# Performance work log

Measured on AMD Instinct MI355X. Metric: run time of the kernel, lower is better.

The kernel has to match this reference:

```python
import jax, jax.numpy as jnp
import numpy as np

H, DH, M, ITERS = 8, 64, 256, 6   # heads, dim_head, num_landmarks, pinv iters
DIM = H * DH                      # 512
KERNEL = 33                       # residual depthwise conv kernel


def setup_inputs() -> dict:
    key = jax.random.key(0)
    ks = jax.random.split(key, 5)
    b, n = 2, 8192                # n multiple of M -> no divisibility padding
    x = jax.random.normal(ks[0], (b, n, DIM), jnp.float32)
    ln_gamma = jnp.ones((DIM,), jnp.float32)
    ln_beta = jnp.zeros((DIM,), jnp.float32)
    w_qkv = jax.random.normal(ks[1], (DIM, 3 * DIM), jnp.float32) * 0.02
    w_out = jax.random.normal(ks[2], (DIM, DIM), jnp.float32) * 0.02
    b_out = jnp.zeros((DIM,), jnp.float32)
    res_kernel = jax.random.normal(ks[3], (H, 1, KERNEL, 1), jnp.float32) * 0.02
    return {"x": x, "ln_gamma": ln_gamma, "ln_beta": ln_beta, "w_qkv": w_qkv,
            "w_out": w_out, "b_out": b_out, "res_kernel": res_kernel}


def _pinv(a, iters):
    # lucidrains moore_penrose_iter_pinv (Newton-Schulz iteration)
    abs_a = jnp.abs(a)
    scale = abs_a.sum(-1).max() * abs_a.sum(-2).max()
    z = jnp.swapaxes(a, -1, -2) / scale
    I = jnp.eye(a.shape[-1], dtype=a.dtype)
    for _ in range(iters):
        az = a @ z
        z = 0.25 * z @ (13.0 * I - az @ (15.0 * I - az @ (7.0 * I - az)))
    return z


def reference(x, ln_gamma, ln_beta, w_qkv, w_out, b_out, res_kernel):
    b, n, d = x.shape
    # pre-LayerNorm (eps 1e-5)
    mu = jnp.mean(x, -1, keepdims=True)
    var = jnp.var(x, -1, keepdims=True)
    xn = (x - mu) * jax.lax.rsqrt(var + 1e-5) * ln_gamma + ln_beta
    # qkv projection (bias-free)
    q, k, v = jnp.split(xn @ w_qkv, 3, axis=-1)
    to_heads = lambda t: t.reshape(b, n, H, DH).transpose(0, 2, 1, 3)  # b h n d
    q, k, v = to_heads(q), to_heads(k), to_heads(v)
    q = q * (DH ** -0.5)
    # landmarks: mean over groups of l consecutive tokens ('(m l) d -> m d')
    l = n // M
    q_l = q.reshape(b, H, M, l, DH).mean(3)  # b h M d
    k_l = k.reshape(b, H, M, l, DH).mean(3)
    sim1 = jnp.einsum('bhnd,bhmd->bhnm', q, k_l)      # queries vs k-landmarks
    sim2 = jnp.einsum('bhid,bhjd->bhij', q_l, k_l)    # landmarks vs landmarks
    sim3 = jnp.einsum('bhmd,bhnd->bhmn', q_l, k)      # q-landmarks vs keys
    a1 = jax.nn.softmax(sim1, axis=-1)
    a2 = jax.nn.softmax(sim2, axis=-1)
    a3 = jax.nn.softmax(sim3, axis=-1)
    a2_inv = _pinv(a2, ITERS)
    out = (a1 @ a2_inv) @ (a3 @ v)  # b h n d
    # residual depthwise conv over the sequence axis (Conv2d kernel (33,1), groups=H)
    pad = KERNEL // 2
    out = out + jax.lax.conv_general_dilated(
        v, res_kernel, (1, 1), [(pad, pad), (0, 0)],
        dimension_numbers=('NCHW', 'OIHW', 'NCHW'), feature_group_count=H)
    out = out.transpose(0, 2, 1, 3).reshape(b, n, d)
    out = out @ w_out + b_out  # to_out Linear (dropout inactive at eval)
    return x + out             # TransLayer residual
```

## Files before the change

kernel.cpp:

```cpp
#include <hip/hip_runtime.h>
#include <math.h>

#define H_ 8
#define DH_ 64
#define DIM_ 512
#define M_ 256
#define N_ 8192
#define BH_ 16
#define LG_ 32
#define KC_ 33
#define PADC_ 16

typedef __attribute__((ext_vector_type(8))) short bf16x8;
typedef __attribute__((ext_vector_type(4))) short s16x4;
typedef __attribute__((ext_vector_type(4))) float f32x4;

__device__ __forceinline__ short f2bf(float f) {
  unsigned u = __float_as_uint(f);
  unsigned r = (u + 0x7FFF + ((u >> 16) & 1)) >> 16;
  return (short)r;
}
__device__ __forceinline__ float bf2f(short s) {
  return __uint_as_float(((unsigned)(unsigned short)s) << 16);
}

__device__ __forceinline__ void mfma_nt_core(const short* __restrict__ A,
                                             const short* __restrict__ Bt, int K,
                                             int m0, int n0, size_t lda, size_t ldb,
                                             f32x4 acc[4][4], short* As, short* Bs) {
  const int tid = threadIdx.x;
  const int wave = tid >> 6, lane = tid & 63;
  const int wr = (wave >> 1) * 64, wc = (wave & 1) * 64;
  const int mi = lane & 15, quad = lane >> 4;
  for (int k0 = 0; k0 < K; k0 += 32) {
#pragma unroll
    for (int t = 0; t < 2; ++t) {
      const int cbase = (t * 4 + wave) * 64;
      const int chunk = cbase + lane;
      const int row = chunk >> 2, cc = (chunk & 3) * 8;
      __builtin_amdgcn_global_load_lds(
          (const __attribute__((address_space(1))) void*)(A + (size_t)(m0 + row) * lda + k0 + cc),
          (__attribute__((address_space(3))) void*)(As + (size_t)cbase * 8), 16, 0, 0);
      __builtin_amdgcn_global_load_lds(
          (const __attribute__((address_space(1))) void*)(Bt + (size_t)(n0 + row) * ldb + k0 + cc),
          (__attribute__((address_space(3))) void*)(Bs + (size_t)cbase * 8), 16, 0, 0);
    }
    __syncthreads();
    bf16x8 af[4], bf[4];
#pragma unroll
    for (int i = 0; i < 4; ++i)
      af[i] = *(const bf16x8*)&As[(wr + i * 16 + mi) * 32 + quad * 8];
#pragma unroll
    for (int j = 0; j < 4; ++j)
      bf[j] = *(const bf16x8*)&Bs[(wc + j * 16 + mi) * 32 + quad * 8];
#pragma unroll
    for (int i = 0; i < 4; ++i)
#pragma unroll
      for (int j = 0; j < 4; ++j)
        acc[i][j] = __builtin_amdgcn_mfma_f32_16x16x32_bf16(af[i], bf[j], acc[i][j], 0, 0, 0);
    __syncthreads();
  }
}

__global__ __launch_bounds__(256) void qkv_mfma(const short* __restrict__ xnb,
                                                const short* __restrict__ wt,
                                                short* __restrict__ qb, short* __restrict__ kb,
                                                short* __restrict__ vb) {
  __shared__ short As[128 * 32], Bs[128 * 32];
  f32x4 acc[4][4] = {};
  const int m0 = blockIdx.x * 128, n0 = blockIdx.y * 128;
  mfma_nt_core(xnb, wt, DIM_, m0, n0, DIM_, DIM_, acc, As, Bs);
  const int wave = threadIdx.x >> 6, lane = threadIdx.x & 63;
  const int wr = (wave >> 1) * 64, wc = (wave & 1) * 64;
  const int mi = lane & 15, quad = lane >> 4;
  const int which = n0 >> 9;
  short* dst = which == 0 ? qb : which == 1 ? kb : vb;
  const float sc = which == 0 ? 0.125f : 1.0f;
#pragma unroll
  for (int j = 0; j < 4; ++j) {
    const int col = n0 + wc + j * 16 + mi;
    const int h = (col >> 6) & 7, d = col & 63;
#pragma unroll
    for (int i = 0; i < 4; ++i) {
#pragma unroll
      for (int r = 0; r < 4; ++r) {
        const int row = m0 + wr + i * 16 + quad * 4 + r;
        const int b = row >> 13, t = row & (N_ - 1);
        dst[((size_t)(b * H_ + h) * N_ + t) * DH_ + d] = f2bf(acc[i][j][r] * sc);
      }
    }
  }
}

__global__ __launch_bounds__(256) void final_mfma(const short* __restrict__ omb,
                                                  const short* __restrict__ wt,
                                                  const float* __restrict__ x,
                                                  const float* __restrict__ bout,
                                                  float* __restrict__ y) {
  __shared__ short As[128 * 32], Bs[128 * 32];
  f32x4 acc[4][4] = {};
  const int m0 = blockIdx.x * 128, n0 = blockIdx.y * 128;
  mfma_nt_core(omb, wt, DIM_, m0, n0, DIM_, DIM_, acc, As, Bs);
  const int wave = threadIdx.x >> 6, lane = threadIdx.x & 63;
  const int wr = (wave >> 1) * 64, wc = (wave & 1) * 64;
  const int mi = lane & 15, quad = lane >> 4;
#pragma unroll
  for (int j = 0; j < 4; ++j) {
    const int col = n0 + wc + j * 16 + mi;
    const float bo = bout[col];
#pragma unroll
    for (int i = 0; i < 4; ++i) {
#pragma unroll
      for (int r = 0; r < 4; ++r) {
        const int row = m0 + wr + i * 16 + quad * 4 + r;
        y[(size_t)row * DIM_ + col] = acc[i][j][r] + x[(size_t)row * DIM_ + col] + bo;
      }
    }
  }
}

__global__ __launch_bounds__(256) void convt_kernel(const float* __restrict__ in,
                                                    short* __restrict__ out, int K, int N) {
  __shared__ float tile[32][33];
  const int n0 = blockIdx.x * 32, k0 = blockIdx.y * 32;
  const int tx = threadIdx.x & 31, ty = threadIdx.x >> 5;
  for (int r = ty; r < 32; r += 8) tile[r][tx] = in[(size_t)(k0 + r) * N + n0 + tx];
  __syncthreads();
  for (int r = ty; r < 32; r += 8) out[(size_t)(n0 + r) * K + k0 + tx] = f2bf(tile[tx][r]);
}

__global__ __launch_bounds__(256) void vt_kernel(const short* __restrict__ vb,
                                                 short* __restrict__ vtb) {
  __shared__ short tile[32][33];
  const int t0 = blockIdx.x * 32, d0 = blockIdx.y * 32, bh = blockIdx.z;
  const int tx = threadIdx.x & 31, ty = threadIdx.x >> 5;
  for (int r = ty; r < 32; r += 8)
    tile[r][tx] = vb[((size_t)bh * N_ + t0 + r) * DH_ + d0 + tx];
  __syncthreads();
  for (int r = ty; r < 32; r += 8)
    vtb[((size_t)bh * DH_ + d0 + r) * N_ + t0 + tx] = tile[tx][r];
}

__global__ __launch_bounds__(128) void ln_kernel(const float* __restrict__ x,
                                                 const float* __restrict__ gamma,
                                                 const float* __restrict__ beta,
                                                 short* __restrict__ xnb) {
  const int row = blockIdx.x, tid = threadIdx.x;
  const float4 v = ((const float4*)(x + (size_t)row * DIM_))[tid];
  float s = v.x + v.y + v.z + v.w;
  float ss = v.x * v.x + v.y * v.y + v.z * v.z + v.w * v.w;
  __shared__ float r1[128], r2[128];
  r1[tid] = s;
  r2[tid] = ss;
  __syncthreads();
  for (int off = 64; off > 0; off >>= 1) {
    if (tid < off) {
      r1[tid] += r1[tid + off];
      r2[tid] += r2[tid + off];
    }
    __syncthreads();
  }
  const float mu = r1[0] * (1.0f / DIM_);
  const float var = r2[0] * (1.0f / DIM_) - mu * mu;
  const float rs = rsqrtf(var + 1e-5f);
  const float4 g = ((const float4*)gamma)[tid];
  const float4 bb = ((const float4*)beta)[tid];
  s16x4 o = {f2bf((v.x - mu) * rs * g.x + bb.x), f2bf((v.y - mu) * rs * g.y + bb.y),
             f2bf((v.z - mu) * rs * g.z + bb.z), f2bf((v.w - mu) * rs * g.w + bb.w)};
  ((s16x4*)(xnb + (size_t)row * DIM_))[tid] = o;
}

__global__ __launch_bounds__(256) void landmark_kernel(const short* __restrict__ qb,
                                                       const short* __restrict__ kb,
                                                       float* __restrict__ ql,
                                                       float* __restrict__ kl,
                                                       short* __restrict__ qlb,
                                                       short* __restrict__ klb) {
  const int idx = blockIdx.x * 256 + threadIdx.x;
  const int d = idx & (DH_ - 1);
  const int m = (idx >> 6) & (M_ - 1);
  const int bh = idx >> 14;
  const size_t base = ((size_t)bh * N_ + m * LG_) * DH_ + d;
  float sq = 0.f, sk = 0.f;
#pragma unroll 8
  for (int t = 0; t < LG_; ++t) {
    sq += bf2f(qb[base + (size_t)t * DH_]);
    sk += bf2f(kb[base + (size_t)t * DH_]);
  }
  sq *= (1.0f / LG_);
  sk *= (1.0f / LG_);
  ql[idx] = sq;
  kl[idx] = sk;
  qlb[idx] = f2bf(sq);
  klb[idx] = f2bf(sk);
}

__global__ __launch_bounds__(256) void sim2_softmax(const float* __restrict__ ql,
                                                    const float* __restrict__ kl,
                                                    float* __restrict__ a2,
                                                    short* __restrict__ a2b) {
  const int i = blockIdx.x, bh = blockIdx.y, j = threadIdx.x;
  __shared__ float qrow[DH_];
  if (j < DH_) qrow[j] = ql[((size_t)bh * M_ + i) * DH_ + j];
  __syncthreads();
  const float* kr = kl + ((size_t)bh * M_ + j) * DH_;
  float s = 0.f;
#pragma unroll 16
  for (int d = 0; d < DH_; ++d) s += qrow[d] * kr[d];
  __shared__ float red[256];
  red[j] = s;
  __syncthreads();
  for (int off = 128; off > 0; off >>= 1) {
    if (j < off) red[j] = fmaxf(red[j], red[j + off]);
    __syncthreads();
  }
  const float mx = red[0];
  __syncthreads();
  const float e = expf(s - mx);
  red[j] = e;
  __syncthreads();
  for (int off = 128; off > 0; off >>= 1) {
    if (j < off) red[j] += red[j + off];
    __syncthreads();
  }
  const float out = e / red[0];
  a2[((size_t)bh * M_ + i) * M_ + j] = out;
  a2b[((size_t)bh * M_ + i) * M_ + j] = f2bf(out);
}

__global__ __launch_bounds__(256) void colmax_kernel(const float* __restrict__ a2,
                                                     unsigned int* __restrict__ scalebits) {
  const int bh = blockIdx.x, j = threadIdx.x;
  const float* mat = a2 + (size_t)bh * M_ * M_;
  float s = 0.f;
  for (int i = 0; i < M_; ++i) s += fabsf(mat[i * M_ + j]);
  __shared__ float red[256];
  red[j] = s;
  __syncthreads();
  for (int off = 128; off > 0; off >>= 1) {
    if (j < off) red[j] = fmaxf(red[j], red[j + off]);
    __syncthreads();
  }
  if (j == 0) atomicMax(scalebits, __float_as_uint(red[0]));
}

__global__ __launch_bounds__(256) void transpose_scale(const float* __restrict__ a2,
                                                       short* __restrict__ z0b,
                                                       const unsigned int* __restrict__ scalebits) {
  const float inv = 1.0f / __uint_as_float(*scalebits);
  const int idx = blockIdx.x * 256 + threadIdx.x;
  const int j = idx & (M_ - 1), i = (idx >> 8) & (M_ - 1), bh = idx >> 16;
  z0b[idx] = f2bf(a2[((size_t)bh * M_ + j) * M_ + i] * inv);
}

__device__ __forceinline__ void ns_core(const short* __restrict__ A, const short* __restrict__ B,
                                        int m0, int n0, short* As, short* Bs, f32x4 acc[4]) {
  const int tid = threadIdx.x, wave = tid >> 6, lane = tid & 63;
  const int mi = lane & 15, quad = lane >> 4;
  const int arow = tid >> 2, acol = (tid & 3) * 8;
  const int bkk = tid & 31, g = tid >> 5;
  for (int k0 = 0; k0 < M_; k0 += 32) {
    __builtin_amdgcn_global_load_lds(
        (const __attribute__((address_space(1))) void*)(A + (size_t)(m0 + arow) * M_ + k0 + acol),
        (__attribute__((address_space(3))) void*)(As + (size_t)wave * 512), 16, 0, 0);
    const bf16x8 bv = *(const bf16x8*)(B + (size_t)(k0 + bkk) * M_ + n0 + g * 8);
#pragma unroll
    for (int e = 0; e < 8; ++e) Bs[(g * 8 + e) * 44 + bkk] = bv[e];
    __syncthreads();
    const bf16x8 af = *(const bf16x8*)&As[(wave * 16 + mi) * 32 + quad * 8];
#pragma unroll
    for (int j = 0; j < 4; ++j) {
      union { bf16x8 v; s16x4 h[2]; } bfr;
      const short* bp = &Bs[(j * 16 + mi) * 44 + quad * 8];
      bfr.h[0] = *(const s16x4*)bp;
      bfr.h[1] = *(const s16x4*)(bp + 4);
      acc[j] = __builtin_amdgcn_mfma_f32_16x16x32_bf16(af, bfr.v, acc[j], 0, 0, 0);
    }
    __syncthreads();
  }
}

__device__ __forceinline__ int ns_remap() {
  const int lin = blockIdx.y * 16 + blockIdx.x;
  return (lin & 7) * (gridDim.y << 1) + (lin >> 3);
}

__global__ __launch_bounds__(256) void ns_gemm0(const short* __restrict__ A,
                                                const short* __restrict__ B,
                                                short* __restrict__ C) {
  __shared__ short As[64 * 32], Bs[64 * 44];
  const int id = ns_remap();
  const int bx = id & 15, by = id >> 4;
  const int m0 = (bx >> 2) * 64, n0 = (bx & 3) * 64;
  const size_t mo = (size_t)by * (M_ * M_);
  f32x4 acc[4] = {};
  ns_core(A + mo, B + mo, m0, n0, As, Bs, acc);
  const int wave = threadIdx.x >> 6, lane = threadIdx.x & 63;
  const int mi = lane & 15, quad = lane >> 4;
#pragma unroll
  for (int j = 0; j < 4; ++j)
#pragma unroll
    for (int r = 0; r < 4; ++r) {
      const int row = m0 + wave * 16 + quad * 4 + r, col = n0 + j * 16 + mi;
      C[mo + (size_t)row * M_ + col] = f2bf(acc[j][r]);
    }
}

__global__ __launch_bounds__(256) void ns_stageA(const short* __restrict__ z,
                                                 const short* __restrict__ y,
                                                 short* __restrict__ p1,
                                                 short* __restrict__ y2,
                                                 short* __restrict__ w) {
  __shared__ short As[64 * 32], Bs[64 * 44];
  const int id = ns_remap();
  const int bx = id & 15, by = id >> 4;
  const int m0 = (bx >> 2) * 64, n0 = (bx & 3) * 64;
  const int sel = by & 1;
  const size_t mo = (size_t)(by >> 1) * (M_ * M_);
  f32x4 acc[4] = {};
  ns_core((sel ? y : z) + mo, y + mo, m0, n0, As, Bs, acc);
  const int wave = threadIdx.x >> 6, lane = threadIdx.x & 63;
  const int mi = lane & 15, quad = lane >> 4;
#pragma unroll
  for (int j = 0; j < 4; ++j)
#pragma unroll
    for (int r = 0; r < 4; ++r) {
      const int row = m0 + wave * 16 + quad * 4 + r, col = n0 + j * 16 + mi;
      const size_t idx = mo + (size_t)row * M_ + col;
      if (sel) {
        y2[idx] = f2bf(acc[j][r]);
        w[idx] = f2bf(1.75f * bf2f(y[idx]) - 0.25f * acc[j][r]);
      } else {
        p1[idx] = f2bf(acc[j][r]);
      }
    }
}

__global__ __launch_bounds__(256) void ns_stageB(const short* __restrict__ p1,
                                                 const short* __restrict__ y2,
                                                 const short* __restrict__ w,
                                                 const short* __restrict__ z,
                                                 const short* __restrict__ y,
                                                 short* __restrict__ zo,
                                                 short* __restrict__ yo,
                                                 float* __restrict__ zf, int zonly) {
  __shared__ short As[64 * 32], Bs[64 * 44];
  const int id = ns_remap();
  const int bx = id & 15, by = id >> 4;
  const int m0 = (bx >> 2) * 64, n0 = (bx & 3) * 64;
  const int sel = zonly ? 0 : (by & 1);
  const size_t mo = (size_t)(zonly ? by : (by >> 1)) * (M_ * M_);
  f32x4 acc[4] = {};
  ns_core((sel ? y2 : p1) + mo, w + mo, m0, n0, As, Bs, acc);
  const int wave = threadIdx.x >> 6, lane = threadIdx.x & 63;
  const int mi = lane & 15, quad = lane >> 4;
#pragma unroll
  for (int j = 0; j < 4; ++j)
#pragma unroll
    for (int r = 0; r < 4; ++r) {
      const int row = m0 + wave * 16 + quad * 4 + r, col = n0 + j * 16 + mi;
      const size_t idx = mo + (size_t)row * M_ + col;
      if (sel) {
        yo[idx] = f2bf(3.25f * bf2f(y[idx]) - 3.75f * bf2f(y2[idx]) + acc[j][r]);
      } else {
        const float v = 3.25f * bf2f(z[idx]) - 3.75f * bf2f(p1[idx]) + acc[j][r];
        zo[idx] = f2bf(v);
        if (zf) zf[idx] = v;
      }
    }
}

__device__ __forceinline__ void mm_step(float (*As)[68], float (*Bs)[68],
                                        int tr, int tc, float acc[4][4]) {
#pragma unroll
  for (int kk = 0; kk < 16; ++kk) {
    const float4 a4 = *(const float4*)&As[kk][tr * 4];
    const float4 b4 = *(const float4*)&Bs[kk][tc * 4];
    const float a[4] = {a4.x, a4.y, a4.z, a4.w};
    const float b[4] = {b4.x, b4.y, b4.z, b4.w};
#pragma unroll
    for (int i = 0; i < 4; ++i)
#pragma unroll
      for (int j = 0; j < 4; ++j) acc[i][j] = fmaf(a[i], b[j], acc[i][j]);
  }
}

__device__ __forceinline__ void load_a_tile(const float* A, int lda, int m0, int k0,
                                            int tid, float (*As)[68]) {
  const int r = tid >> 2, kq = tid & 3;
  const float4 a4 = *(const float4*)(A + (size_t)(m0 + r) * lda + k0 + kq * 4);
  As[kq * 4 + 0][r] = a4.x;
  As[kq * 4 + 1][r] = a4.y;
  As[kq * 4 + 2][r] = a4.z;
  As[kq * 4 + 3][r] = a4.w;
}

__device__ __forceinline__ void load_b_nn(const float* B, int ldb, int k0, int n0,
                                          int tid, float (*Bs)[68]) {
  const int kr = tid >> 4, c4 = tid & 15;
  const float4 b4 = *(const float4*)(B + (size_t)(k0 + kr) * ldb + n0 + c4 * 4);
  *(float4*)&Bs[kr][c4 * 4] = b4;
}

__global__ __launch_bounds__(256) void gemm_nn64(const float* __restrict__ A, int lda,
                                                 long long strideA,
                                                 const float* __restrict__ B, long long strideB,
                                                 float* __restrict__ C, long long strideC,
                                                 int kchunk) {
  const int bz = blockIdx.z;
  A += (size_t)bz * strideA;
  B += (size_t)bz * strideB;
  C += (size_t)bz * strideC;
  const int m0 = blockIdx.x * 64;
  const int tid = threadIdx.x, tr = tid >> 4, tc = tid & 15;
  __shared__ float As[16][68], Bs[16][68];
  float acc[4][4] = {};
  for (int k0 = 0; k0 < kchunk; k0 += 16) {
    load_a_tile(A, lda, m0, k0, tid, As);
    load_b_nn(B, DH_, k0, 0, tid, Bs);
    __syncthreads();
    mm_step(As, Bs, tr, tc, acc);
    __syncthreads();
  }
#pragma unroll
  for (int i = 0; i < 4; ++i) {
    const int row = m0 + tr * 4 + i;
    *(float4*)(C + (size_t)row * DH_ + tc * 4) =
        make_float4(acc[i][0], acc[i][1], acc[i][2], acc[i][3]);
  }
}

__global__ __launch_bounds__(256) void a3_flash(const short* __restrict__ qlb,
                                                const short* __restrict__ kb,
                                                const short* __restrict__ vtb,
                                                float* __restrict__ Opart,
                                                float* __restrict__ mpart,
                                                float* __restrict__ lpart) {
  const int chunk = blockIdx.x, rt = blockIdx.y, bh = blockIdx.z;
  __shared__ short qs[64 * 80], ks[64 * 80], ps[64 * 80];
  const int tid = threadIdx.x, wave = tid >> 6, lane = tid & 63;
  const int mi = lane & 15, quad = lane >> 4;
#pragma unroll
  for (int i = 0; i < 2; ++i) {
    const int c = tid * 2 + i, row = c >> 3, col = (c & 7) * 8;
    *(bf16x8*)&qs[row * 80 + col] =
        *(const bf16x8*)(qlb + ((size_t)bh * M_ + rt * 64 + row) * DH_ + col);
  }
  __syncthreads();
  const bf16x8 aq0 = *(const bf16x8*)&qs[(wave * 16 + mi) * 80 + quad * 8];
  const bf16x8 aq1 = *(const bf16x8*)&qs[(wave * 16 + mi) * 80 + 32 + quad * 8];
  float m[4] = {-INFINITY, -INFINITY, -INFINITY, -INFINITY};
  float l[4] = {0.f, 0.f, 0.f, 0.f};
  f32x4 o[4] = {};
  for (int t = 0; t < 16; ++t) {
    const int n0 = chunk * 1024 + t * 64;
#pragma unroll
    for (int i = 0; i < 2; ++i) {
      const int c = tid * 2 + i, row = c >> 3, col = (c & 7) * 8;
      *(bf16x8*)&ks[row * 80 + col] =
          *(const bf16x8*)(kb + ((size_t)bh * N_ + n0 + row) * DH_ + col);
    }
    __syncthreads();
    f32x4 s[4];
#pragma unroll
    for (int j = 0; j < 4; ++j) {
      const bf16x8 b0 = *(const bf16x8*)&ks[(j * 16 + mi) * 80 + quad * 8];
      const bf16x8 b1 = *(const bf16x8*)&ks[(j * 16 + mi) * 80 + 32 + quad * 8];
      f32x4 z = {0.f, 0.f, 0.f, 0.f};
      z = __builtin_amdgcn_mfma_f32_16x16x32_bf16(aq0, b0, z, 0, 0, 0);
      s[j] = __builtin_amdgcn_mfma_f32_16x16x32_bf16(aq1, b1, z, 0, 0, 0);
    }
    float alpha[4];
#pragma unroll
    for (int r = 0; r < 4; ++r) {
      float v = fmaxf(fmaxf(s[0][r], s[1][r]), fmaxf(s[2][r], s[3][r]));
      v = fmaxf(v, __shfl_xor(v, 1, 64));
      v = fmaxf(v, __shfl_xor(v, 2, 64));
      v = fmaxf(v, __shfl_xor(v, 4, 64));
      v = fmaxf(v, __shfl_xor(v, 8, 64));
      const float mnew = fmaxf(m[r], v);
      alpha[r] = __expf(m[r] - mnew);
      m[r] = mnew;
    }
    float rs[4] = {0.f, 0.f, 0.f, 0.f};
#pragma unroll
    for (int j = 0; j < 4; ++j)
#pragma unroll
      for (int r = 0; r < 4; ++r) {
        const float p = __expf(s[j][r] - m[r]);
        rs[r] += p;
        ps[(wave * 16 + quad * 4 + r) * 80 + j * 16 + mi] = f2bf(p);
      }
#pragma unroll
    for (int r = 0; r < 4; ++r) {
      float v = rs[r];
      v += __shfl_xor(v, 1, 64);
      v += __shfl_xor(v, 2, 64);
      v += __shfl_xor(v, 4, 64);
      v += __shfl_xor(v, 8, 64);
      l[r] = l[r] * alpha[r] + v;
#pragma unroll
      for (int j = 0; j < 4; ++j) o[j][r] *= alpha[r];
    }
    __syncthreads();
    const bf16x8 ap0 = *(const bf16x8*)&ps[(wave * 16 + mi) * 80 + quad * 8];
    const bf16x8 ap1 = *(const bf16x8*)&ps[(wave * 16 + mi) * 80 + 32 + quad * 8];
#pragma unroll
    for (int j = 0; j < 4; ++j) {
      const short* vp = vtb + ((size_t)bh * DH_ + j * 16 + mi) * N_ + n0;
      const bf16x8 b0 = *(const bf16x8*)(vp + quad * 8);
      const bf16x8 b1 = *(const bf16x8*)(vp + 32 + quad * 8);
      o[j] = __builtin_amdgcn_mfma_f32_16x16x32_bf16(ap0, b0, o[j], 0, 0, 0);
      o[j] = __builtin_amdgcn_mfma_f32_16x16x32_bf16(ap1, b1, o[j], 0, 0, 0);
    }
    __syncthreads();
  }
  const int p2 = bh * 4 + rt;
  float* Ob = Opart + ((size_t)chunk * 64 + p2) * 4096;
#pragma unroll
  for (int j = 0; j < 4; ++j)
#pragma unroll
    for (int r = 0; r < 4; ++r)
      Ob[(wave * 16 + quad * 4 + r) * 64 + j * 16 + mi] = o[j][r];
  if (mi == 0) {
#pragma unroll
    for (int r = 0; r < 4; ++r) {
      mpart[((size_t)chunk * 64 + p2) * 64 + wave * 16 + quad * 4 + r] = m[r];
      lpart[((size_t)chunk * 64 + p2) * 64 + wave * 16 + quad * 4 + r] = l[r];
    }
  }
}

__global__ __launch_bounds__(256) void a3_combine(const float* __restrict__ Opart,
                                                  const float* __restrict__ mpart,
                                                  const float* __restrict__ lpart,
                                                  float* __restrict__ a3v) {
  const int p2 = blockIdx.x;
  const int bh = p2 >> 2, rt = p2 & 3;
  __shared__ float wgt[8][64];
  const int tid = threadIdx.x;
  if (tid < 64) {
    float mg = -INFINITY;
    for (int c = 0; c < 8; ++c) mg = fmaxf(mg, mpart[((size_t)c * 64 + p2) * 64 + tid]);
    float e[8], lg = 0.f;
    for (int c = 0; c < 8; ++c) {
      e[c] = __expf(mpart[((size_t)c * 64 + p2) * 64 + tid] - mg);
      lg += lpart[((size_t)c * 64 + p2) * 64 + tid] * e[c];
    }
    const float inv = 1.f / lg;
    for (int c = 0; c < 8; ++c) wgt[c][tid] = e[c] * inv;
  }
  __syncthreads();
  for (int i = tid; i < 4096; i += 256) {
    const int row = i >> 6, d = i & 63;
    float s = 0.f;
    for (int c = 0; c < 8; ++c) s += Opart[((size_t)c * 64 + p2) * 4096 + i] * wgt[c][row];
    a3v[((size_t)bh * M_ + rt * 64 + row) * DH_ + d] = s;
  }
}

__global__ __launch_bounds__(256) void w2t_kernel(const float* __restrict__ w2,
                                                  short* __restrict__ w2tb) {
  const int bh = blockIdx.x, tid = threadIdx.x;
  for (int i = tid; i < M_ * DH_; i += 256) {
    const int r = i >> 6, d = i & 63;
    w2tb[((size_t)bh * DH_ + d) * M_ + r] = f2bf(w2[(size_t)bh * M_ * DH_ + i]);
  }
}

__global__ __launch_bounds__(256, 5) void a1_conv(const short* __restrict__ qb,
                                                  const short* __restrict__ klb,
                                                  const short* __restrict__ w2tb,
                                                  const short* __restrict__ vtb,
                                                  const float* __restrict__ rk,
                                                  short* __restrict__ omb) {
  __shared__ __align__(16) char smem[20096];
  short* kls = (short*)smem;
  short* ps = (short*)smem;
  short* vwin = (short*)smem;
  short* band = (short*)(smem + 17920);
  const int bh = blockIdx.y, t0 = blockIdx.x * 64;
  const int b = bh >> 3, h = bh & 7;
  const int tid = threadIdx.x, wave = tid >> 6, lane = tid & 63;
  const int mi = lane & 15, quad = lane >> 4;

  const short* qrow = qb + ((size_t)bh * N_ + t0 + wave * 16 + mi) * DH_;
  const bf16x8 aq0 = *(const bf16x8*)(qrow + quad * 8);
  const bf16x8 aq1 = *(const bf16x8*)(qrow + 32 + quad * 8);

#pragma unroll
  for (int i = 0; i < 4; ++i) {
    const int idx = tid + i * 256;
    const int r = idx >> 6, c = idx & 63, u = c - r;
    band[r * 68 + c] = (u >= 0 && u < KC_) ? f2bf(rk[h * KC_ + u]) : (short)0;
  }

  f32x4 s[16] = {};
#pragma unroll
  for (int half = 0; half < 2; ++half) {
    if (half) __syncthreads();
#pragma unroll
    for (int i = 0; i < 4; ++i) {
      const int cb = i * 256 + wave * 64;
      const int c = cb + lane;
      const int row = c >> 3, cc = c & 7;
      __builtin_amdgcn_global_load_lds(
          (const __attribute__((address_space(1))) void*)(
              klb + ((size_t)bh * M_ + half * 128 + row) * DH_ + (cc ^ (row & 7)) * 8),
          (__attribute__((address_space(3))) void*)(kls + (size_t)cb * 8), 16, 0, 0);
    }
    __syncthreads();
#pragma unroll
    for (int f = 0; f < 8; ++f) {
      const int row = f * 16 + mi;
      const bf16x8 blo = *(const bf16x8*)&kls[row * 64 + ((quad ^ (row & 7)) * 8)];
      const bf16x8 bhi = *(const bf16x8*)&kls[row * 64 + (((quad + 4) ^ (row & 7)) * 8)];
      f32x4 z = __builtin_amdgcn_mfma_f32_16x16x32_bf16(aq0, blo, s[half * 8 + f], 0, 0, 0);
      s[half * 8 + f] = __builtin_amdgcn_mfma_f32_16x16x32_bf16(aq1, bhi, z, 0, 0, 0);
    }
  }
  float inv[4];
#pragma unroll
  for (int r = 0; r < 4; ++r) {
    float v = s[0][r];
#pragma unroll
    for (int f = 1; f < 16; ++f) v = fmaxf(v, s[f][r]);
    v = fmaxf(v, __shfl_xor(v, 1, 64));
    v = fmaxf(v, __shfl_xor(v, 2, 64));
    v = fmaxf(v, __shfl_xor(v, 4, 64));
    v = fmaxf(v, __shfl_xor(v, 8, 64));
    float sum = 0.f;
#pragma unroll
    for (int f = 0; f < 16; ++f) {
      const float p = __expf(s[f][r] - v);
      s[f][r] = p;
      sum += p;
    }
    sum += __shfl_xor(sum, 1, 64);
    sum += __shfl_xor(sum, 2, 64);
    sum += __shfl_xor(sum, 4, 64);
    sum += __shfl_xor(sum, 8, 64);
    inv[r] = 1.f / sum;
  }
  __syncthreads();

  f32x4 o[4] = {};
#pragma unroll
  for (int half = 0; half < 2; ++half) {
#pragma unroll
    for (int f = 0; f < 8; ++f)
#pragma unroll
      for (int r = 0; r < 4; ++r)
        ps[(wave * 16 + quad * 4 + r) * 140 + f * 16 + mi] = f2bf(s[half * 8 + f][r] * inv[r]);
#pragma unroll
    for (int k0 = 0; k0 < 4; ++k0) {
      union { bf16x8 v; s16x4 hh[2]; } ap;
      const short* pp = &ps[(wave * 16 + mi) * 140 + k0 * 32 + quad * 8];
      ap.hh[0] = *(const s16x4*)pp;
      ap.hh[1] = *(const s16x4*)(pp + 4);
#pragma unroll
      for (int j = 0; j < 4; ++j) {
        const bf16x8 bw = *(const bf16x8*)(w2tb + ((size_t)bh * DH_ + j * 16 + mi) * M_ +
                                           (half * 4 + k0) * 32 + quad * 8);
        o[j] = __builtin_amdgcn_mfma_f32_16x16x32_bf16(ap.v, bw, o[j], 0, 0, 0);
      }
    }
  }
  __syncthreads();

  {
    const int d = tid & 63, cg0 = tid >> 6;
    const short* vrow = vtb + ((size_t)bh * DH_ + d) * N_;
    for (int ch = cg0; ch < 14; ch += 4) {
      const int tbase = t0 - 16 + ch * 8;
      bf16x8 vv;
      if (tbase >= 0 && tbase + 8 <= N_) {
        vv = *(const bf16x8*)(vrow + tbase);
      } else {
#pragma unroll
        for (int e = 0; e < 8; ++e) {
          const int tt = tbase + e;
          vv[e] = (tt >= 0 && tt < N_) ? vrow[tt] : (short)0;
        }
      }
      *(bf16x8*)&vwin[d * 116 + ch * 8] = vv;
    }
  }
  __syncthreads();

#pragma unroll
  for (int ks = 0; ks < 2; ++ks) {
    union { bf16x8 v; s16x4 hh[2]; } ab;
    const short* bp = &band[mi * 68 + ks * 32 + quad * 8];
    ab.hh[0] = *(const s16x4*)bp;
    ab.hh[1] = *(const s16x4*)(bp + 4);
#pragma unroll
    for (int j = 0; j < 4; ++j) {
      union { bf16x8 v; s16x4 hh[2]; } bv;
      const short* vp = &vwin[(j * 16 + mi) * 116 + wave * 16 + ks * 32 + quad * 8];
      bv.hh[0] = *(const s16x4*)vp;
      bv.hh[1] = *(const s16x4*)(vp + 4);
      o[j] = __builtin_amdgcn_mfma_f32_16x16x32_bf16(ab.v, bv.v, o[j], 0, 0, 0);
    }
  }
#pragma unroll
  for (int j = 0; j < 4; ++j) {
    const int d = j * 16 + mi;
#pragma unroll
    for (int r = 0; r < 4; ++r) {
      const int t = t0 + wave * 16 + quad * 4 + r;
      omb[((size_t)(b * N_ + t)) * DIM_ + h * DH_ + d] = f2bf(o[j][r]);
    }
  }
}

extern "C" void kernel_launch(void* const* d_in, const int* in_sizes, int n_in,
                              void* d_out, int out_size, void* d_ws, size_t ws_size,
                              hipStream_t stream) {
  (void)in_sizes; (void)n_in; (void)out_size;
  const float* x = (const float*)d_in[0];
  const float* gamma = (const float*)d_in[1];
  const float* beta = (const float*)d_in[2];
  const float* wqkv = (const float*)d_in[3];
  const float* wout = (const float*)d_in[4];
  const float* bout = (const float*)d_in[5];
  const float* rk = (const float*)d_in[6];
  float* y = (float*)d_out;
  float* ws = (float*)d_ws;

  size_t o = 0;
  short* xnb = (short*)(ws + o);   o += (size_t)2 * N_ * DIM_ / 2;
  short* wqkvt = (short*)(ws + o); o += (size_t)3 * DIM_ * DIM_ / 2;
  short* woutt = (short*)(ws + o); o += (size_t)DIM_ * DIM_ / 2;
  short* qb = (short*)(ws + o);    o += (size_t)BH_ * N_ * DH_ / 2;
  short* kb = (short*)(ws + o);    o += (size_t)BH_ * N_ * DH_ / 2;
  short* vb = (short*)(ws + o);    o += (size_t)BH_ * N_ * DH_ / 2;
  short* vtb = (short*)(ws + o);   o += (size_t)BH_ * N_ * DH_ / 2;
  float* ql = ws + o;  o += (size_t)BH_ * M_ * DH_;
  float* kl = ws + o;  o += (size_t)BH_ * M_ * DH_;
  short* qlb = (short*)(ws + o); o += (size_t)BH_ * M_ * DH_ / 2;
  short* klb = (short*)(ws + o); o += (size_t)BH_ * M_ * DH_ / 2;
  float* a2 = ws + o;  o += (size_t)BH_ * M_ * M_;
  float* z0f = ws + o; o += (size_t)BH_ * M_ * M_;
  short* a2b = (short*)(ws + o); o += (size_t)BH_ * M_ * M_ / 2;
  short* zb0 = (short*)(ws + o); o += (size_t)BH_ * M_ * M_ / 2;
  short* zb1 = (short*)(ws + o); o += (size_t)BH_ * M_ * M_ / 2;
  short* yb0 = (short*)(ws + o); o += (size_t)BH_ * M_ * M_ / 2;
  short* yb1 = (short*)(ws + o); o += (size_t)BH_ * M_ * M_ / 2;
  short* p1b = (short*)(ws + o); o += (size_t)BH_ * M_ * M_ / 2;
  short* y2b = (short*)(ws + o); o += (size_t)BH_ * M_ * M_ / 2;
  short* wb  = (short*)(ws + o); o += (size_t)BH_ * M_ * M_ / 2;
  float* Opart = ws + o; o += (size_t)8 * 64 * 4096;
  float* mpart = ws + o; o += (size_t)8 * 64 * 64;
  float* lpart = ws + o; o += (size_t)8 * 64 * 64;
  float* a3v = ws + o; o += (size_t)BH_ * M_ * DH_;
  float* w2 = ws + o;  o += (size_t)BH_ * M_ * DH_;
  short* w2tb = (short*)(ws + o); o += (size_t)BH_ * M_ * DH_ / 2;
  short* omb = (short*)(ws + o);  o += (size_t)2 * N_ * DIM_ / 2;
  unsigned int* scalebits = (unsigned int*)(ws + o); o += 16;
  if (ws_size < o * sizeof(float)) return;

  (void)hipMemsetAsync(scalebits, 0, 64, stream);
  ln_kernel<<<2 * N_, 128, 0, stream>>>(x, gamma, beta, xnb);
  convt_kernel<<<dim3(3 * DIM_ / 32, DIM_ / 32), 256, 0, stream>>>(wqkv, wqkvt, DIM_, 3 * DIM_);
  convt_kernel<<<dim3(DIM_ / 32, DIM_ / 32), 256, 0, stream>>>(wout, woutt, DIM_, DIM_);
  qkv_mfma<<<dim3(2 * N_ / 128, 3 * DIM_ / 128), 256, 0, stream>>>(xnb, wqkvt, qb, kb, vb);
  vt_kernel<<<dim3(N_ / 32, 2, BH_), 256, 0, stream>>>(vb, vtb);

  landmark_kernel<<<BH_ * M_ * DH_ / 256, 256, 0, stream>>>(qb, kb, ql, kl, qlb, klb);
  sim2_softmax<<<dim3(M_, BH_), 256, 0, stream>>>(ql, kl, a2, a2b);
  colmax_kernel<<<BH_, 256, 0, stream>>>(a2, scalebits);
  transpose_scale<<<BH_ * M_ * M_ / 256, 256, 0, stream>>>(a2, zb0, scalebits);

  a3_flash<<<dim3(8, 4, BH_), 256, 0, stream>>>(qlb, kb, vtb, Opart, mpart, lpart);
  a3_combine<<<64, 256, 0, stream>>>(Opart, mpart, lpart, a3v);

  ns_gemm0<<<dim3(16, BH_), 256, 0, stream>>>(a2b, zb0, yb0);
  short* zc = zb0; short* zn = zb1; short* yc = yb0; short* yn = yb1;
  for (int it = 0; it < 6; ++it) {
    const int last = (it == 5);
    ns_stageA<<<dim3(16, 2 * BH_), 256, 0, stream>>>(zc, yc, p1b, y2b, wb);
    ns_stageB<<<dim3(16, last ? BH_ : 2 * BH_), 256, 0, stream>>>(
        p1b, y2b, wb, zc, yc, zn, yn, last ? z0f : nullptr, last);
    short* t;
    t = zc; zc = zn; zn = t;
    t = yc; yc = yn; yn = t;
  }

  gemm_nn64<<<dim3(M_ / 64, 1, BH_), 256, 0, stream>>>(
      z0f, M_, (long long)M_ * M_, a3v, (long long)M_ * DH_, w2, (long long)M_ * DH_, M_);
  w2t_kernel<<<BH_, 256, 0, stream>>>(w2, w2tb);

  a1_conv<<<dim3(N_ / 64, BH_), 256, 0, stream>>>(qb, klb, w2tb, vtb, rk, omb);

  final_mfma<<<dim3(2 * N_ / 128, DIM_ / 128), 256, 0, stream>>>(omb, woutt, x, bout, y);
}
```

Before: 474.9 us.

## Split a3 flash into more chunks, async-stage swizzled K, online softmax in a1_conv

The a3 flash-attention kernel now uses twice as many sequence chunks, each doing half the tiles, so more blocks run in parallel. K tiles are staged through asynchronous global-to-LDS loads into an XOR-swizzled unpadded layout, and the next tile is prefetched while softmax runs. The combine kernel is widened to match. a1_conv switches from a full two-pass softmax held in 16 score registers to an online softmax per half, which lowers register pressure, and drops its occupancy hint. In exchange there is more partial-result traffic in the combine step and extra rescaling work.

```diff
diff --git a/kernel.cpp b/kernel.cpp
--- a/kernel.cpp
+++ b/kernel.cpp
@@ -9,7 +9,8 @@
 #define BH_ 16
 #define LG_ 32
 #define KC_ 33
-#define PADC_ 16
+#define CH_ 16
+#define NTI_ 8
 
 typedef __attribute__((ext_vector_type(8))) short bf16x8;
 typedef __attribute__((ext_vector_type(4))) short s16x4;
@@ -430,6 +431,20 @@
   }
 }
 
+__device__ __forceinline__ void stage_ks(const short* __restrict__ kb, int bh, int n0,
+                                         int wave, int lane, short* ks) {
+#pragma unroll
+  for (int i = 0; i < 2; ++i) {
+    const int cb = i * 256 + wave * 64;
+    const int c = cb + lane;
+    const int row = c >> 3, cc = c & 7;
+    __builtin_amdgcn_global_load_lds(
+        (const __attribute__((address_space(1))) void*)(
+            kb + ((size_t)bh * N_ + n0 + row) * DH_ + ((cc ^ (row & 7)) * 8)),
+        (__attribute__((address_space(3))) void*)(ks + (size_t)cb * 8), 16, 0, 0);
+  }
+}
+
 __global__ __launch_bounds__(256) void a3_flash(const short* __restrict__ qlb,
                                                 const short* __restrict__ kb,
                                                 const short* __restrict__ vtb,
@@ -437,39 +452,32 @@
                                                 float* __restrict__ mpart,
                                                 float* __restrict__ lpart) {
   const int chunk = blockIdx.x, rt = blockIdx.y, bh = blockIdx.z;
-  __shared__ short qs[64 * 80], ks[64 * 80], ps[64 * 80];
+  __shared__ short ks[64 * 64];
+  __shared__ short ps[64 * 64];
   const int tid = threadIdx.x, wave = tid >> 6, lane = tid & 63;
   const int mi = lane & 15, quad = lane >> 4;
-#pragma unroll
-  for (int i = 0; i < 2; ++i) {
-    const int c = tid * 2 + i, row = c >> 3, col = (c & 7) * 8;
-    *(bf16x8*)&qs[row * 80 + col] =
-        *(const bf16x8*)(qlb + ((size_t)bh * M_ + rt * 64 + row) * DH_ + col);
-  }
-  __syncthreads();
-  const bf16x8 aq0 = *(const bf16x8*)&qs[(wave * 16 + mi) * 80 + quad * 8];
-  const bf16x8 aq1 = *(const bf16x8*)&qs[(wave * 16 + mi) * 80 + 32 + quad * 8];
+  const short* qrow = qlb + ((size_t)bh * M_ + rt * 64 + wave * 16 + mi) * DH_;
+  const bf16x8 aq0 = *(const bf16x8*)(qrow + quad * 8);
+  const bf16x8 aq1 = *(const bf16x8*)(qrow + 32 + quad * 8);
   float m[4] = {-INFINITY, -INFINITY, -INFINITY, -INFINITY};
   float l[4] = {0.f, 0.f, 0.f, 0.f};
   f32x4 o[4] = {};
-  for (int t = 0; t < 16; ++t) {
-    const int n0 = chunk * 1024 + t * 64;
-#pragma unroll
-    for (int i = 0; i < 2; ++i) {
-      const int c = tid * 2 + i, row = c >> 3, col = (c & 7) * 8;
-      *(bf16x8*)&ks[row * 80 + col] =
-          *(const bf16x8*)(kb + ((size_t)bh * N_ + n0 + row) * DH_ + col);
-    }
-    __syncthreads();
+  stage_ks(kb, bh, chunk * (N_ / CH_), wave, lane, ks);
+  __syncthreads();
+  for (int t = 0; t < NTI_; ++t) {
+    const int n0 = chunk * (N_ / CH_) + t * 64;
     f32x4 s[4];
 #pragma unroll
     for (int j = 0; j < 4; ++j) {
-      const bf16x8 b0 = *(const bf16x8*)&ks[(j * 16 + mi) * 80 + quad * 8];
-      const bf16x8 b1 = *(const bf16x8*)&ks[(j * 16 + mi) * 80 + 32 + quad * 8];
+      const int row = j * 16 + mi;
+      const bf16x8 b0 = *(const bf16x8*)&ks[row * 64 + ((quad ^ (row & 7)) * 8)];
+      const bf16x8 b1 = *(const bf16x8*)&ks[row * 64 + (((quad + 4) ^ (row & 7)) * 8)];
       f32x4 z = {0.f, 0.f, 0.f, 0.f};
       z = __builtin_amdgcn_mfma_f32_16x16x32_bf16(aq0, b0, z, 0, 0, 0);
       s[j] = __builtin_amdgcn_mfma_f32_16x16x32_bf16(aq1, b1, z, 0, 0, 0);
     }
+    __syncthreads();
+    if (t + 1 < NTI_) stage_ks(kb, bh, n0 + 64, wave, lane, ks);
     float alpha[4];
 #pragma unroll
     for (int r = 0; r < 4; ++r) {
@@ -489,7 +497,9 @@
       for (int r = 0; r < 4; ++r) {
         const float p = __expf(s[j][r] - m[r]);
         rs[r] += p;
-        ps[(wave * 16 + quad * 4 + r) * 80 + j * 16 + mi] = f2bf(p);
+        const int prow = wave * 16 + quad * 4 + r;
+        const int pcol = j * 16 + mi;
+        ps[prow * 64 + (((pcol >> 3) ^ (prow & 7)) * 8) + (pcol & 7)] = f2bf(p);
       }
 #pragma unroll
     for (int r = 0; r < 4; ++r) {
@@ -502,9 +512,9 @@
 #pragma unroll
       for (int j = 0; j < 4; ++j) o[j][r] *= alpha[r];
     }
-    __syncthreads();
-    const bf16x8 ap0 = *(const bf16x8*)&ps[(wave * 16 + mi) * 80 + quad * 8];
-    const bf16x8 ap1 = *(const bf16x8*)&ps[(wave * 16 + mi) * 80 + 32 + quad * 8];
+    const int prow = wave * 16 + mi;
+    const bf16x8 ap0 = *(const bf16x8*)&ps[prow * 64 + ((quad ^ (mi & 7)) * 8)];
+    const bf16x8 ap1 = *(const bf16x8*)&ps[prow * 64 + (((quad + 4) ^ (mi & 7)) * 8)];
 #pragma unroll
     for (int j = 0; j < 4; ++j) {
       const short* vp = vtb + ((size_t)bh * DH_ + j * 16 + mi) * N_ + n0;
@@ -535,26 +545,30 @@
                                                   const float* __restrict__ mpart,
                                                   const float* __restrict__ lpart,
                                                   float* __restrict__ a3v) {
-  const int p2 = blockIdx.x;
+  const int p2 = blockIdx.x, ds = blockIdx.y;
   const int bh = p2 >> 2, rt = p2 & 3;
-  __shared__ float wgt[8][64];
+  __shared__ float wgt[CH_][64];
   const int tid = threadIdx.x;
   if (tid < 64) {
     float mg = -INFINITY;
-    for (int c = 0; c < 8; ++c) mg = fmaxf(mg, mpart[((size_t)c * 64 + p2) * 64 + tid]);
-    float e[8], lg = 0.f;
-    for (int c = 0; c < 8; ++c) {
+#pragma unroll
+    for (int c = 0; c < CH_; ++c) mg = fmaxf(mg, mpart[((size_t)c * 64 + p2) * 64 + tid]);
+    float e[CH_], lg = 0.f;
+#pragma unroll
+    for (int c = 0; c < CH_; ++c) {
       e[c] = __expf(mpart[((size_t)c * 64 + p2) * 64 + tid] - mg);
       lg += lpart[((size_t)c * 64 + p2) * 64 + tid] * e[c];
     }
     const float inv = 1.f / lg;
-    for (int c = 0; c < 8; ++c) wgt[c][tid] = e[c] * inv;
-  }
-  __syncthreads();
-  for (int i = tid; i < 4096; i += 256) {
+#pragma unroll
+    for (int c = 0; c < CH_; ++c) wgt[c][tid] = e[c] * inv;
+  }
+  __syncthreads();
+  for (int i = ds * 1024 + tid; i < ds * 1024 + 1024; i += 256) {
     const int row = i >> 6, d = i & 63;
     float s = 0.f;
-    for (int c = 0; c < 8; ++c) s += Opart[((size_t)c * 64 + p2) * 4096 + i] * wgt[c][row];
+#pragma unroll
+    for (int c = 0; c < CH_; ++c) s += Opart[((size_t)c * 64 + p2) * 4096 + i] * wgt[c][row];
     a3v[((size_t)bh * M_ + rt * 64 + row) * DH_ + d] = s;
   }
 }
@@ -568,12 +582,12 @@
   }
 }
 
-__global__ __launch_bounds__(256, 5) void a1_conv(const short* __restrict__ qb,
-                                                  const short* __restrict__ klb,
-                                                  const short* __restrict__ w2tb,
-                                                  const short* __restrict__ vtb,
-                                                  const float* __restrict__ rk,
-                                                  short* __restrict__ omb) {
+__global__ __launch_bounds__(256) void a1_conv(const short* __restrict__ qb,
+                                               const short* __restrict__ klb,
+                                               const short* __restrict__ w2tb,
+                                               const short* __restrict__ vtb,
+                                               const float* __restrict__ rk,
+                                               short* __restrict__ omb) {
   __shared__ __align__(16) char smem[20096];
   short* kls = (short*)smem;
   short* ps = (short*)smem;
@@ -595,7 +609,9 @@
     band[r * 68 + c] = (u >= 0 && u < KC_) ? f2bf(rk[h * KC_ + u]) : (short)0;
   }
 
-  f32x4 s[16] = {};
+  float m[4] = {-INFINITY, -INFINITY, -INFINITY, -INFINITY};
+  float l[4] = {0.f, 0.f, 0.f, 0.f};
+  f32x4 o[4] = {};
 #pragma unroll
   for (int half = 0; half < 2; ++half) {
     if (half) __syncthreads();
@@ -610,48 +626,50 @@
           (__attribute__((address_space(3))) void*)(kls + (size_t)cb * 8), 16, 0, 0);
     }
     __syncthreads();
+    f32x4 s[8];
 #pragma unroll
     for (int f = 0; f < 8; ++f) {
       const int row = f * 16 + mi;
       const bf16x8 blo = *(const bf16x8*)&kls[row * 64 + ((quad ^ (row & 7)) * 8)];
       const bf16x8 bhi = *(const bf16x8*)&kls[row * 64 + (((quad + 4) ^ (row & 7)) * 8)];
-      f32x4 z = __builtin_amdgcn_mfma_f32_16x16x32_bf16(aq0, blo, s[half * 8 + f], 0, 0, 0);
-      s[half * 8 + f] = __builtin_amdgcn_mfma_f32_16x16x32_bf16(aq1, bhi, z, 0, 0, 0);
-    }
-  }
-  float inv[4];
-#pragma unroll
-  for (int r = 0; r < 4; ++r) {
-    float v = s[0][r];
-#pragma unroll
-    for (int f = 1; f < 16; ++f) v = fmaxf(v, s[f][r]);
-    v = fmaxf(v, __shfl_xor(v, 1, 64));
-    v = fmaxf(v, __shfl_xor(v, 2, 64));
-    v = fmaxf(v, __shfl_xor(v, 4, 64));
-    v = fmaxf(v, __shfl_xor(v, 8, 64));
-    float sum = 0.f;
-#pragma unroll
-    for (int f = 0; f < 16; ++f) {
-      const float p = __expf(s[f][r] - v);
-      s[f][r] = p;
-      sum += p;
-    }
-    sum += __shfl_xor(sum, 1, 64);
-    sum += __shfl_xor(sum, 2, 64);
-    sum += __shfl_xor(sum, 4, 64);
-    sum += __shfl_xor(sum, 8, 64);
-    inv[r] = 1.f / sum;
-  }
-  __syncthreads();
-
-  f32x4 o[4] = {};
-#pragma unroll
-  for (int half = 0; half < 2; ++half) {
+      f32x4 z = {0.f, 0.f, 0.f, 0.f};
+      z = __builtin_amdgcn_mfma_f32_16x16x32_bf16(aq0, blo, z, 0, 0, 0);
+      s[f] = __builtin_amdgcn_mfma_f32_16x16x32_bf16(aq1, bhi, z, 0, 0, 0);
+    }
+    __syncthreads();
+#pragma unroll
+    for (int r = 0; r < 4; ++r) {
+      float v = s[0][r];
+#pragma unroll
+      for (int f = 1; f < 8; ++f) v = fmaxf(v, s[f][r]);
+      v = fmaxf(v, __shfl_xor(v, 1, 64));
+      v = fmaxf(v, __shfl_xor(v, 2, 64));
+      v = fmaxf(v, __shfl_xor(v, 4, 64));
+      v = fmaxf(v, __shfl_xor(v, 8, 64));
+      const float mnew = fmaxf(m[r], v);
+      const float alpha = __expf(m[r] - mnew);
+      m[r] = mnew;
+      l[r] *= alpha;
+#pragma unroll
+      for (int j = 0; j < 4; ++j) o[j][r] *= alpha;
+      float sum = 0.f;
+#pragma unroll
+      for (int f = 0; f < 8; ++f) {
+        const float p = __expf(s[f][r] - mnew);
+        s[f][r] = p;
+        sum += p;
+      }
+      sum += __shfl_xor(sum, 1, 64);
+      sum += __shfl_xor(sum, 2, 64);
+      sum += __shfl_xor(sum, 4, 64);
+      sum += __shfl_xor(sum, 8, 64);
+      l[r] += sum;
+    }
 #pragma unroll
     for (int f = 0; f < 8; ++f)
 #pragma unroll
       for (int r = 0; r < 4; ++r)
-        ps[(wave * 16 + quad * 4 + r) * 140 + f * 16 + mi] = f2bf(s[half * 8 + f][r] * inv[r]);
+        ps[(wave * 16 + quad * 4 + r) * 140 + f * 16 + mi] = f2bf(s[f][r]);
 #pragma unroll
     for (int k0 = 0; k0 < 4; ++k0) {
       union { bf16x8 v; s16x4 hh[2]; } ap;
@@ -687,6 +705,13 @@
     }
   }
   __syncthreads();
+
+#pragma unroll
+  for (int r = 0; r < 4; ++r) {
+    const float inv = 1.f / l[r];
+#pragma unroll
+    for (int j = 0; j < 4; ++j) o[j][r] *= inv;
+  }
 
 #pragma unroll
   for (int ks = 0; ks < 2; ++ks) {
@@ -750,9 +775,9 @@
   short* p1b = (short*)(ws + o); o += (size_t)BH_ * M_ * M_ / 2;
   short* y2b = (short*)(ws + o); o += (size_t)BH_ * M_ * M_ / 2;
   short* wb  = (short*)(ws + o); o += (size_t)BH_ * M_ * M_ / 2;
-  float* Opart = ws + o; o += (size_t)8 * 64 * 4096;
-  float* mpart = ws + o; o += (size_t)8 * 64 * 64;
-  float* lpart = ws + o; o += (size_t)8 * 64 * 64;
+  float* Opart = ws + o; o += (size_t)CH_ * 64 * 4096;
+  float* mpart = ws + o; o += (size_t)CH_ * 64 * 64;
+  float* lpart = ws + o; o += (size_t)CH_ * 64 * 64;
   float* a3v = ws + o; o += (size_t)BH_ * M_ * DH_;
   float* w2 = ws + o;  o += (size_t)BH_ * M_ * DH_;
   short* w2tb = (short*)(ws + o); o += (size_t)BH_ * M_ * DH_ / 2;
@@ -772,8 +797,8 @@
   colmax_kernel<<<BH_, 256, 0, stream>>>(a2, scalebits);
   transpose_scale<<<BH_ * M_ * M_ / 256, 256, 0, stream>>>(a2, zb0, scalebits);
 
-  a3_flash<<<dim3(8, 4, BH_), 256, 0, stream>>>(qlb, kb, vtb, Opart, mpart, lpart);
-  a3_combine<<<64, 256, 0, stream>>>(Opart, mpart, lpart, a3v);
+  a3_flash<<<dim3(CH_, 4, BH_), 256, 0, stream>>>(qlb, kb, vtb, Opart, mpart, lpart);
+  a3_combine<<<dim3(64, 4), 256, 0, stream>>>(Opart, mpart, lpart, a3v);
 
   ns_gemm0<<<dim3(16, BH_), 256, 0, stream>>>(a2b, zb0, yb0);
   short* zc = zb0; short* zn = zb1; short* yc = yb0; short* yn = yb1;
```

New measurement: 469.7 us. Within noise of the previous version (-1.1%).
